# Performance work log

Measured on AMD Instinct MI355X. Metric: run time of the kernel, lower is better.

Reference implementation:

```python
import jax, jax.numpy as jnp
import numpy as np

B, I, R, A, V = 256, 512, 512, 196, 10000

def _linear_params(key, out_dim, in_dim):
    k1, k2 = jax.random.split(key)
    s = 1.0 / np.sqrt(in_dim)
    W = jax.random.uniform(k1, (out_dim, in_dim), minval=-s, maxval=s, dtype=jnp.float32)
    b = jax.random.uniform(k2, (out_dim,), minval=-s, maxval=s, dtype=jnp.float32)
    return W, b

def setup_inputs() -> dict:
    key = jax.random.key(0)
    ks = jax.random.split(key, 16)
    d = {}
    d['x'] = jax.random.normal(ks[0], (B, I), dtype=jnp.float32)
    d['att'] = jax.random.normal(ks[1], (B, A, R), dtype=jnp.float32)
    d['prev_c'] = jax.random.normal(ks[2], (B, R), dtype=jnp.float32)
    d['prev_h'] = jax.random.normal(ks[3], (B, R), dtype=jnp.float32)
    for i, (name, o, inn) in enumerate([('a2a', A, R), ('h2a', A, R), ('d2d', 1, A),
                                         ('i2h', 4 * R, I), ('a2h', 4 * R, R), ('h2h', 4 * R, R),
                                         ('a2a1', A, R), ('h2a1', A, R), ('d2d1', 1, A),
                                         ('proj', V, R)]):
        W, b = _linear_params(ks[4 + i], o, inn)
        d['W_' + name] = W
        d['b_' + name] = b
    return d

def _lin(x, W, b):
    return x @ W.T + b

def _attend(att, h, Wa, ba, Wh, bh, Wd, bd):
    # att: (B, A, R); h: (B, R)
    av = jnp.einsum('bar,or->bao', att, Wa) + ba        # (B, A, A)
    ah = _lin(h, Wh, bh)                                # (B, A)
    dot = jnp.tanh(av + ah[:, :, None])                 # (B, A, A)
    scores = jnp.einsum('bao,o->ba', dot, Wd[0]) + bd[0]  # (B, A)
    w = jax.nn.softmax(scores, axis=-1)
    return jnp.einsum('bar,ba->br', att, w)             # (B, R)

def reference(x, att, prev_c, prev_h,
              W_a2a, b_a2a, W_h2a, b_h2a, W_d2d, b_d2d,
              W_i2h, b_i2h, W_a2h, b_a2h, W_h2h, b_h2h,
              W_a2a1, b_a2a1, W_h2a1, b_h2a1, W_d2d1, b_d2d1,
              W_proj, b_proj):
    # first attention uses prev_h
    prev_att_res = _attend(att, prev_h, W_a2a, b_a2a, W_h2a, b_h2a, W_d2d, b_d2d)
    sums = _lin(x, W_i2h, b_i2h) + _lin(prev_h, W_h2h, b_h2h) + _lin(prev_att_res, W_a2h, b_a2h)
    sig = jax.nn.sigmoid(sums[:, :3 * R])
    in_gate = sig[:, 0:R]
    forget_gate = sig[:, R:2 * R]
    out_gate = sig[:, 2 * R:3 * R]
    in_transform = jnp.tanh(sums[:, 3 * R:4 * R])
    next_c = forget_gate * prev_c + in_gate * in_transform
    next_h = out_gate * jnp.tanh(next_c)
    # second attention uses next_h
    att_res = _attend(att, next_h, W_a2a1, b_a2a1, W_h2a1, b_h2a1, W_d2d1, b_d2d1)
    top_h = att_res + next_h
    logsoft = jax.nn.log_softmax(_lin(top_h, W_proj, b_proj), axis=-1)
    return next_c, top_h, logsoft
```

## Files before the change

kernel.cpp:

```cpp
#include <hip/hip_runtime.h>
#include <math.h>

constexpr int cB  = 256;
constexpr int cI  = 512;
constexpr int cR  = 512;
constexpr int cA  = 196;
constexpr int cV  = 10000;
constexpr int cH4 = 2048;
constexpr int AV2_LD = 200;

typedef short bf16x8 __attribute__((ext_vector_type(8)));
typedef float f32x4  __attribute__((ext_vector_type(4)));
typedef unsigned short us8 __attribute__((ext_vector_type(8)));

__device__ inline unsigned short f2bf(float f) {
    unsigned int u = __float_as_uint(f);
    u += 0x7fffu + ((u >> 16) & 1u);
    return (unsigned short)(u >> 16);
}
__device__ inline float bf2f(unsigned short s) {
    return __uint_as_float(((unsigned int)s) << 16);
}
__device__ inline float tanh_f(float x) {
    return 1.f - 2.f / (1.f + __expf(2.f * x));
}

__global__ __launch_bounds__(256) void k_cvt_ah(
    const float* __restrict__ s0, unsigned short* __restrict__ d0, int nb0,
    const float* __restrict__ s1, unsigned short* __restrict__ d1, int nb1,
    const float* __restrict__ s2, unsigned short* __restrict__ d2, int nb2,
    const float* __restrict__ s3, unsigned short* __restrict__ d3, int nb3,
    const float* __restrict__ h, const float* __restrict__ W,
    const float* __restrict__ bias, float* __restrict__ outah)
{
    __shared__ __align__(16) float h_s[cR];
    int blk = blockIdx.x;
    int ncvt = nb0 + nb1 + nb2 + nb3;
    int t = threadIdx.x;
    if (blk < ncvt) {
        const float* src; unsigned short* dst; int base;
        if (blk < nb0)                  { src = s0; dst = d0; base = blk; }
        else if (blk < nb0 + nb1)       { src = s1; dst = d1; base = blk - nb0; }
        else if (blk < nb0 + nb1 + nb2) { src = s2; dst = d2; base = blk - nb0 - nb1; }
        else                            { src = s3; dst = d3; base = blk - nb0 - nb1 - nb2; }
        int i = base * 256 + t;
        float4 v = ((const float4*)src)[i];
        ushort4 b;
        b.x = f2bf(v.x); b.y = f2bf(v.y); b.z = f2bf(v.z); b.w = f2bf(v.w);
        ((ushort4*)dst)[i] = b;
    } else {
        int b = blk - ncvt;
        h_s[t]       = h[b * cR + t];
        h_s[t + 256] = h[b * cR + t + 256];
        __syncthreads();
        if (t < cA) {
            const float4* Wv = (const float4*)(W + (size_t)t * cR);
            const float4* hv = (const float4*)h_s;
            float acc = 0.f;
            #pragma unroll 4
            for (int k = 0; k < cR / 4; ++k) {
                float4 w4 = Wv[k], x4 = hv[k];
                acc += w4.x * x4.x + w4.y * x4.y + w4.z * x4.z + w4.w * x4.w;
            }
            outah[b * cA + t] = acc + bias[t];
        }
    }
}

__global__ __launch_bounds__(256) void k_ah(
    const float* __restrict__ h, const float* __restrict__ W,
    const float* __restrict__ bias, float* __restrict__ out)
{
    __shared__ __align__(16) float h_s[cR];
    int b = blockIdx.x;
    int t = threadIdx.x;
    h_s[t]       = h[b * cR + t];
    h_s[t + 256] = h[b * cR + t + 256];
    __syncthreads();
    if (t < cA) {
        const float4* Wv = (const float4*)(W + (size_t)t * cR);
        const float4* hv = (const float4*)h_s;
        float acc = 0.f;
        #pragma unroll 4
        for (int k = 0; k < cR / 4; ++k) {
            float4 w4 = Wv[k], x4 = hv[k];
            acc += w4.x * x4.x + w4.y * x4.y + w4.z * x4.z + w4.w * x4.w;
        }
        out[b * cA + t] = acc + bias[t];
    }
}

constexpr int SC_LDA = 72;

__global__ __launch_bounds__(512, 2) void k_scores2g(
    const float* __restrict__ att, unsigned short* __restrict__ att_bf,
    const unsigned short* __restrict__ wa1_bf,
    const unsigned short* __restrict__ wa2_bf,
    const float* __restrict__ ba1, const float* __restrict__ ba2,
    const float* __restrict__ Wd1, const float* __restrict__ bd1,
    const float* __restrict__ ah, float* __restrict__ scores,
    unsigned short* __restrict__ av2)
{
    __shared__ __align__(16) unsigned short att_s[128][SC_LDA];
    __shared__ __align__(16) unsigned short wa_s[448][SC_LDA];
    __shared__ float ba1_s[224];
    __shared__ float ba2_s[224];
    __shared__ float wd_s[224];
    __shared__ float part_s[128][2];

    int tid  = threadIdx.x;
    int wave = tid >> 6;
    int lane = tid & 63;
    int lx   = lane & 15;
    int quad = lane >> 4;
    int mg   = wave >> 2;
    int ng   = wave & 3;
    size_t row0 = (size_t)blockIdx.x * 128;

    if (tid < 224) {
        ba1_s[tid] = (tid < cA) ? ba1[tid] : 0.f;
        ba2_s[tid] = (tid < cA) ? ba2[tid] : 0.f;
        wd_s[tid]  = (tid < cA) ? Wd1[tid] : 0.f;
    }

    int a_r = tid >> 4, a_c = (tid & 15) * 4;
    int w_r = tid >> 3, w_c = (tid & 7) * 8;
    const float* attA = att + (row0 + a_r) * cR + a_c;
    unsigned short* wbA = att_bf + (row0 + a_r) * cR + a_c;

    f32x4 acc[4][7];
    #pragma unroll
    for (int m = 0; m < 4; ++m)
        #pragma unroll
        for (int c = 0; c < 7; ++c) acc[m][c] = (f32x4){0.f, 0.f, 0.f, 0.f};

    float4 patt[4];
    us8    pwa[7];
    #pragma unroll
    for (int i = 0; i < 4; ++i)
        patt[i] = *(const float4*)(attA + (size_t)i * 32 * cR);
    #pragma unroll
    for (int i = 0; i < 7; ++i) {
        int R = w_r + 64 * i;
        const unsigned short* src = (R < 224) ? wa1_bf : wa2_bf;
        int rr = (R < 224) ? R : R - 224;
        pwa[i] = (rr < cA) ? *(const us8*)(src + (size_t)rr * cR + w_c)
                           : (us8){0,0,0,0,0,0,0,0};
    }

    for (int k0 = 0; k0 < cR; k0 += 64) {
        #pragma unroll
        for (int i = 0; i < 4; ++i) {
            float4 v = patt[i];
            ushort4 bv;
            bv.x = f2bf(v.x); bv.y = f2bf(v.y); bv.z = f2bf(v.z); bv.w = f2bf(v.w);
            *(ushort4*)&att_s[a_r + 32 * i][a_c] = bv;
            *(ushort4*)(wbA + (size_t)i * 32 * cR + k0) = bv;
        }
        #pragma unroll
        for (int i = 0; i < 7; ++i)
            *(us8*)&wa_s[w_r + 64 * i][w_c] = pwa[i];
        if (k0 + 64 < cR) {
            #pragma unroll
            for (int i = 0; i < 4; ++i)
                patt[i] = *(const float4*)(attA + (size_t)i * 32 * cR + k0 + 64);
            #pragma unroll
            for (int i = 0; i < 7; ++i) {
                int R = w_r + 64 * i;
                const unsigned short* src = (R < 224) ? wa1_bf : wa2_bf;
                int rr = (R < 224) ? R : R - 224;
                pwa[i] = (rr < cA) ? *(const us8*)(src + (size_t)rr * cR + k0 + 64 + w_c)
                                   : (us8){0,0,0,0,0,0,0,0};
            }
        }
        __syncthreads();
        #pragma unroll
        for (int ks = 0; ks < 2; ++ks) {
            int kb = ks * 32 + quad * 8;
            bf16x8 af[4];
            #pragma unroll
            for (int m = 0; m < 4; ++m)
                af[m] = *(const bf16x8*)&att_s[mg * 64 + m * 16 + lx][kb];
            #pragma unroll
            for (int c = 0; c < 7; ++c) {
                bf16x8 bfr = *(const bf16x8*)&wa_s[ng * 112 + c * 16 + lx][kb];
                #pragma unroll
                for (int m = 0; m < 4; ++m)
                    acc[m][c] = __builtin_amdgcn_mfma_f32_16x16x32_bf16(af[m], bfr, acc[m][c], 0, 0, 0);
            }
        }
        __syncthreads();
    }

    if (ng < 2) {
        #pragma unroll
        for (int m = 0; m < 4; ++m) {
            #pragma unroll
            for (int reg = 0; reg < 4; ++reg) {
                int rl = mg * 64 + m * 16 + quad * 4 + reg;
                float ahv = ah[row0 + rl];
                float part = 0.f;
                #pragma unroll
                for (int c = 0; c < 7; ++c) {
                    int col = ng * 112 + c * 16 + lx;
                    part += tanh_f(acc[m][c][reg] + ba1_s[col] + ahv) * wd_s[col];
                }
                part += __shfl_xor(part, 1);
                part += __shfl_xor(part, 2);
                part += __shfl_xor(part, 4);
                part += __shfl_xor(part, 8);
                if (lx == 0) part_s[rl][ng] = part;
            }
        }
    } else {
        int cb = (ng - 2) * 112;
        #pragma unroll
        for (int m = 0; m < 4; ++m) {
            #pragma unroll
            for (int reg = 0; reg < 4; ++reg) {
                int rl = mg * 64 + m * 16 + quad * 4 + reg;
                size_t ro = (size_t)(row0 + rl) * AV2_LD;
                #pragma unroll
                for (int c = 0; c < 7; ++c) {
                    int col = cb + c * 16 + lx;
                    float v = acc[m][c][reg] + ba2_s[col];
                    if (col < cA)          av2[ro + col] = f2bf(v);
                    else if (col < AV2_LD) av2[ro + col] = 0;
                }
            }
        }
    }
    __syncthreads();
    if (tid < 128)
        scores[row0 + tid] = part_s[tid][0] + part_s[tid][1] + bd1[0];
}

__global__ __launch_bounds__(256) void k_dot2(
    const unsigned short* __restrict__ av2, const float* __restrict__ ah,
    const float* __restrict__ Wd, const float* __restrict__ bd,
    float* __restrict__ scores)
{
    __shared__ float wd_s[AV2_LD];
    int t = threadIdx.x;
    if (t < AV2_LD) wd_s[t] = (t < cA) ? Wd[t] : 0.f;
    __syncthreads();
    int wave = t >> 6, half = (t >> 5) & 1, L = t & 31;
    int r = blockIdx.x * 8 + wave * 2 + half;
    int b = r / cA;
    float s = 0.f;
    if (L < 25) {
        us8 v = *(const us8*)(av2 + (size_t)r * AV2_LD + L * 8);
        const float* ap = ah + (size_t)b * cA + L * 8;
        float4 a0 = *(const float4*)(ap);
        float4 a1 = (L < 24) ? *(const float4*)(ap + 4)
                             : make_float4(0.f, 0.f, 0.f, 0.f);
        float av[8] = {a0.x, a0.y, a0.z, a0.w, a1.x, a1.y, a1.z, a1.w};
        #pragma unroll
        for (int j = 0; j < 8; ++j)
            s += tanh_f(bf2f(v[j]) + av[j]) * wd_s[L * 8 + j];
    }
    s += __shfl_xor(s, 1);
    s += __shfl_xor(s, 2);
    s += __shfl_xor(s, 4);
    s += __shfl_xor(s, 8);
    s += __shfl_xor(s, 16);
    if (L == 0) scores[r] = s + bd[0];
}

__global__ __launch_bounds__(256, 2) void k_scores_cv(
    const float* __restrict__ att, unsigned short* __restrict__ att_bf,
    const unsigned short* __restrict__ wa_bf,
    const float* __restrict__ ba, const float* __restrict__ Wd,
    const float* __restrict__ bd, const float* __restrict__ ah,
    float* __restrict__ scores, int wb)
{
    __shared__ __align__(16) unsigned short att_s[128][SC_LDA];
    __shared__ __align__(16) unsigned short wa_s[224][SC_LDA];
    __shared__ float ba_s[224];
    __shared__ float wd_s[224];
    __shared__ float part_s[128][2];

    int tid  = threadIdx.x;
    int wave = tid >> 6;
    int lane = tid & 63;
    int lx   = lane & 15;
    int quad = lane >> 4;
    int mg   = wave >> 1;
    int ng   = wave & 1;
    size_t row0 = (size_t)blockIdx.x * 128;

    if (tid < 224) {
        ba_s[tid] = (tid < cA) ? ba[tid] : 0.f;
        wd_s[tid] = (tid < cA) ? Wd[tid] : 0.f;
    }

    int a_r = tid >> 4, a_c = (tid & 15) * 4;
    int w_r = tid >> 3, w_c = (tid & 7) * 8;
    const float* attA = att + (row0 + a_r) * cR + a_c;
    unsigned short* wbA = att_bf + (row0 + a_r) * cR + a_c;

    f32x4 acc[4][7];
    #pragma unroll
    for (int m = 0; m < 4; ++m)
        #pragma unroll
        for (int c = 0; c < 7; ++c) acc[m][c] = (f32x4){0.f, 0.f, 0.f, 0.f};

    float4 patt[8];
    us8    pwa[7];
    #pragma unroll
    for (int i = 0; i < 8; ++i)
        patt[i] = *(const float4*)(attA + (size_t)i * 16 * cR);
    #pragma unroll
    for (int i = 0; i < 7; ++i) {
        int r = w_r + 32 * i;
        pwa[i] = (r < cA) ? *(const us8*)(wa_bf + (size_t)r * cR + w_c)
                          : (us8){0,0,0,0,0,0,0,0};
    }

    for (int k0 = 0; k0 < cR; k0 += 64) {
        #pragma unroll
        for (int i = 0; i < 8; ++i) {
            float4 v = patt[i];
            ushort4 bv;
            bv.x = f2bf(v.x); bv.y = f2bf(v.y); bv.z = f2bf(v.z); bv.w = f2bf(v.w);
            *(ushort4*)&att_s[a_r + 16 * i][a_c] = bv;
            if (wb)
                *(ushort4*)(wbA + (size_t)i * 16 * cR + k0) = bv;
        }
        #pragma unroll
        for (int i = 0; i < 7; ++i)
            *(us8*)&wa_s[w_r + 32 * i][w_c] = pwa[i];
        if (k0 + 64 < cR) {
            #pragma unroll
            for (int i = 0; i < 8; ++i)
                patt[i] = *(const float4*)(attA + (size_t)i * 16 * cR + k0 + 64);
            #pragma unroll
            for (int i = 0; i < 7; ++i) {
                int r = w_r + 32 * i;
                pwa[i] = (r < cA) ? *(const us8*)(wa_bf + (size_t)r * cR + k0 + 64 + w_c)
                                  : (us8){0,0,0,0,0,0,0,0};
            }
        }
        __syncthreads();
        #pragma unroll
        for (int ks = 0; ks < 2; ++ks) {
            int kb = ks * 32 + quad * 8;
            bf16x8 af[4];
            #pragma unroll
            for (int m = 0; m < 4; ++m)
                af[m] = *(const bf16x8*)&att_s[mg * 64 + m * 16 + lx][kb];
            #pragma unroll
            for (int c = 0; c < 7; ++c) {
                bf16x8 bfr = *(const bf16x8*)&wa_s[ng * 112 + c * 16 + lx][kb];
                #pragma unroll
                for (int m = 0; m < 4; ++m)
                    acc[m][c] = __builtin_amdgcn_mfma_f32_16x16x32_bf16(af[m], bfr, acc[m][c], 0, 0, 0);
            }
        }
        __syncthreads();
    }

    #pragma unroll
    for (int m = 0; m < 4; ++m) {
        #pragma unroll
        for (int reg = 0; reg < 4; ++reg) {
            int rl = mg * 64 + m * 16 + quad * 4 + reg;
            float ahv = ah[row0 + rl];
            float part = 0.f;
            #pragma unroll
            for (int c = 0; c < 7; ++c) {
                int col = ng * 112 + c * 16 + lx;
                part += tanh_f(acc[m][c][reg] + ba_s[col] + ahv) * wd_s[col];
            }
            part += __shfl_xor(part, 1);
            part += __shfl_xor(part, 2);
            part += __shfl_xor(part, 4);
            part += __shfl_xor(part, 8);
            if (lx == 0) part_s[rl][ng] = part;
        }
    }
    __syncthreads();
    if (tid < 128)
        scores[row0 + tid] = part_s[tid][0] + part_s[tid][1] + bd[0];
}

__global__ __launch_bounds__(256, 2) void k_scores_bf(
    const unsigned short* __restrict__ att_bf,
    const unsigned short* __restrict__ wa_bf,
    const float* __restrict__ ba, const float* __restrict__ Wd,
    const float* __restrict__ bd, const float* __restrict__ ah,
    float* __restrict__ scores)
{
    __shared__ __align__(16) unsigned short att_s[128][SC_LDA];
    __shared__ __align__(16) unsigned short wa_s[224][SC_LDA];
    __shared__ float ba_s[224];
    __shared__ float wd_s[224];
    __shared__ float part_s[128][2];

    int tid  = threadIdx.x;
    int wave = tid >> 6;
    int lane = tid & 63;
    int lx   = lane & 15;
    int quad = lane >> 4;
    int mg   = wave >> 1;
    int ng   = wave & 1;
    size_t row0 = (size_t)blockIdx.x * 128;

    if (tid < 224) {
        ba_s[tid] = (tid < cA) ? ba[tid] : 0.f;
        wd_s[tid] = (tid < cA) ? Wd[tid] : 0.f;
    }

    int a_r = tid >> 3, a_c = (tid & 7) * 8;
    int w_r = tid >> 3, w_c = (tid & 7) * 8;
    const unsigned short* attA = att_bf + (row0 + a_r) * cR + a_c;

    f32x4 acc[4][7];
    #pragma unroll
    for (int m = 0; m < 4; ++m)
        #pragma unroll
        for (int c = 0; c < 7; ++c) acc[m][c] = (f32x4){0.f, 0.f, 0.f, 0.f};

    us8 patt[4];
    us8 pwa[7];
    #pragma unroll
    for (int i = 0; i < 4; ++i)
        patt[i] = *(const us8*)(attA + (size_t)i * 32 * cR);
    #pragma unroll
    for (int i = 0; i < 7; ++i) {
        int r = w_r + 32 * i;
        pwa[i] = (r < cA) ? *(const us8*)(wa_bf + (size_t)r * cR + w_c)
                          : (us8){0,0,0,0,0,0,0,0};
    }

    for (int k0 = 0; k0 < cR; k0 += 64) {
        #pragma unroll
        for (int i = 0; i < 4; ++i)
            *(us8*)&att_s[a_r + 32 * i][a_c] = patt[i];
        #pragma unroll
        for (int i = 0; i < 7; ++i)
            *(us8*)&wa_s[w_r + 32 * i][w_c] = pwa[i];
        if (k0 + 64 < cR) {
            #pragma unroll
            for (int i = 0; i < 4; ++i)
                patt[i] = *(const us8*)(attA + (size_t)i * 32 * cR + k0 + 64);
            #pragma unroll
            for (int i = 0; i < 7; ++i) {
                int r = w_r + 32 * i;
                pwa[i] = (r < cA) ? *(const us8*)(wa_bf + (size_t)r * cR + k0 + 64 + w_c)
                                  : (us8){0,0,0,0,0,0,0,0};
            }
        }
        __syncthreads();
        #pragma unroll
        for (int ks = 0; ks < 2; ++ks) {
            int kb = ks * 32 + quad * 8;
            bf16x8 af[4];
            #pragma unroll
            for (int m = 0; m < 4; ++m)
                af[m] = *(const bf16x8*)&att_s[mg * 64 + m * 16 + lx][kb];
            #pragma unroll
            for (int c = 0; c < 7; ++c) {
                bf16x8 bfr = *(const bf16x8*)&wa_s[ng * 112 + c * 16 + lx][kb];
                #pragma unroll
                for (int m = 0; m < 4; ++m)
                    acc[m][c] = __builtin_amdgcn_mfma_f32_16x16x32_bf16(af[m], bfr, acc[m][c], 0, 0, 0);
            }
        }
        __syncthreads();
    }

    #pragma unroll
    for (int m = 0; m < 4; ++m) {
        #pragma unroll
        for (int reg = 0; reg < 4; ++reg) {
            int rl = mg * 64 + m * 16 + quad * 4 + reg;
            float ahv = ah[row0 + rl];
            float part = 0.f;
            #pragma unroll
            for (int c = 0; c < 7; ++c) {
                int col = ng * 112 + c * 16 + lx;
                part += tanh_f(acc[m][c][reg] + ba_s[col] + ahv) * wd_s[col];
            }
            part += __shfl_xor(part, 1);
            part += __shfl_xor(part, 2);
            part += __shfl_xor(part, 4);
            part += __shfl_xor(part, 8);
            if (lx == 0) part_s[rl][ng] = part;
        }
    }
    __syncthreads();
    if (tid < 128)
        scores[row0 + tid] = part_s[tid][0] + part_s[tid][1] + bd[0];
}

__device__ inline void softmax_w(const float* scores, int b, int t, float* red,
                                 float* w_s)
{
    float s = (t < cA) ? scores[b * cA + t] : -INFINITY;
    red[t] = s; __syncthreads();
    for (int off = 128; off > 0; off >>= 1) {
        if (t < off) red[t] = fmaxf(red[t], red[t + off]);
        __syncthreads();
    }
    float mx = red[0];
    __syncthreads();
    float e = (t < cA) ? __expf(s - mx) : 0.f;
    red[t] = e; __syncthreads();
    for (int off = 128; off > 0; off >>= 1) {
        if (t < off) red[t] += red[t + off];
        __syncthreads();
    }
    float inv = 1.f / red[0];
    if (t < cA) w_s[t] = e * inv;
    __syncthreads();
}

__global__ __launch_bounds__(512) void k_attres_bf(
    const float* __restrict__ scores, const unsigned short* __restrict__ att_bf,
    const float* __restrict__ addin,
    float* __restrict__ out, unsigned short* __restrict__ out_bf)
{
    __shared__ float red[512];
    __shared__ float w_s[cA];
    __shared__ float red2[8][512];
    int b = blockIdx.x, t = threadIdx.x;

    float s = (t < cA) ? scores[b * cA + t] : -INFINITY;
    red[t] = s; __syncthreads();
    for (int off = 256; off > 0; off >>= 1) {
        if (t < off) red[t] = fmaxf(red[t], red[t + off]);
        __syncthreads();
    }
    float mx = red[0];
    __syncthreads();
    float e = (t < cA) ? __expf(s - mx) : 0.f;
    red[t] = e; __syncthreads();
    for (int off = 256; off > 0; off >>= 1) {
        if (t < off) red[t] += red[t + off];
        __syncthreads();
    }
    float inv = 1.f / red[0];
    if (t < cA) w_s[t] = e * inv;
    __syncthreads();

    int p = t >> 6, l = t & 63;
    const unsigned short* base = att_bf + (size_t)b * cA * cR + l * 8;
    float acc[8] = {};
    #pragma unroll 4
    for (int a = p; a < cA; a += 8) {
        us8 v = *(const us8*)(base + (size_t)a * cR);
        float w = w_s[a];
        #pragma unroll
        for (int j = 0; j < 8; ++j)
            acc[j] += bf2f(v[j]) * w;
    }
    #pragma unroll
    for (int j = 0; j < 8; ++j)
        red2[p][l * 8 + j] = acc[j];
    __syncthreads();
    {
        int r = t;
        float s2 = red2[0][r] + red2[1][r] + red2[2][r] + red2[3][r]
                 + red2[4][r] + red2[5][r] + red2[6][r] + red2[7][r];
        if (addin) s2 += addin[b * cR + r];
        out[b * cR + r] = s2;
        out_bf[b * cR + r] = f2bf(s2);
    }
}

__global__ __launch_bounds__(256) void k_attres_f32(
    const float* __restrict__ scores, const float* __restrict__ att,
    const float* __restrict__ addin,
    float* __restrict__ out, unsigned short* __restrict__ out_bf)
{
    __shared__ float red[256];
    __shared__ float w_s[cA];
    int b = blockIdx.x, t = threadIdx.x;
    softmax_w(scores, b, t, red, w_s);

    const float* attb = att + (size_t)b * cA * cR + 2 * t;
    float acc0 = 0.f, acc1 = 0.f;
    #pragma unroll 4
    for (int a = 0; a < cA; ++a) {
        float2 u = *(const float2*)(attb + (size_t)a * cR);
        float w = w_s[a];
        acc0 += u.x * w;
        acc1 += u.y * w;
    }
    if (addin) {
        acc0 += addin[b * cR + 2 * t];
        acc1 += addin[b * cR + 2 * t + 1];
    }
    out[b * cR + 2 * t]     = acc0;
    out[b * cR + 2 * t + 1] = acc1;
    out_bf[b * cR + 2 * t]     = f2bf(acc0);
    out_bf[b * cR + 2 * t + 1] = f2bf(acc1);
}

__global__ __launch_bounds__(256, 4) void k_sums(
    const unsigned short* __restrict__ x_bf,
    const unsigned short* __restrict__ h_bf,
    const unsigned short* __restrict__ ar_bf,
    const float* __restrict__ Wi, const float* __restrict__ Wh,
    const float* __restrict__ Wa,
    const float* __restrict__ bi, const float* __restrict__ bh,
    const float* __restrict__ ba, float* __restrict__ out)
{
    __shared__ __align__(16) unsigned short a_s[32][SC_LDA];
    __shared__ __align__(16) unsigned short w_s[64][SC_LDA];
    int tid  = threadIdx.x;
    int wave = tid >> 6;
    int lane = tid & 63;
    int lx   = lane & 15;
    int quad = lane >> 4;
    int b0 = blockIdx.x * 32;
    int j0 = blockIdx.y * 64;

    const unsigned short* Aarr[3] = {x_bf, h_bf, ar_bf};
    const float* Warr[3] = {Wi, Wh, Wa};

    int a_r = tid >> 3, a_c = (tid & 7) * 8;
    int w_r = tid >> 4, w_c = (tid & 15) * 4;

    f32x4 acc0 = {0.f, 0.f, 0.f, 0.f}, acc1 = {0.f, 0.f, 0.f, 0.f};

    us8 pa;
    float4 pw[4];
    pa = *(const us8*)(Aarr[0] + (size_t)(b0 + a_r) * cR + a_c);
    #pragma unroll
    for (int i = 0; i < 4; ++i)
        pw[i] = *(const float4*)(Warr[0] + (size_t)(j0 + w_r + 16 * i) * cR + w_c);

    for (int it = 0; it < 24; ++it) {
        *(us8*)&a_s[a_r][a_c] = pa;
        #pragma unroll
        for (int i = 0; i < 4; ++i) {
            float4 v = pw[i];
            ushort4 bv;
            bv.x = f2bf(v.x); bv.y = f2bf(v.y); bv.z = f2bf(v.z); bv.w = f2bf(v.w);
            *(ushort4*)&w_s[w_r + 16 * i][w_c] = bv;
        }
        if (it < 23) {
            int s2 = (it + 1) >> 3, k2 = ((it + 1) & 7) * 64;
            pa = *(const us8*)(Aarr[s2] + (size_t)(b0 + a_r) * cR + k2 + a_c);
            #pragma unroll
            for (int i = 0; i < 4; ++i)
                pw[i] = *(const float4*)(Warr[s2] + (size_t)(j0 + w_r + 16 * i) * cR + k2 + w_c);
        }
        __syncthreads();
        #pragma unroll
        for (int ks = 0; ks < 2; ++ks) {
            int kb = ks * 32 + quad * 8;
            bf16x8 afr0 = *(const bf16x8*)&a_s[lx][kb];
            bf16x8 afr1 = *(const bf16x8*)&a_s[16 + lx][kb];
            bf16x8 bfr  = *(const bf16x8*)&w_s[wave * 16 + lx][kb];
            acc0 = __builtin_amdgcn_mfma_f32_16x16x32_bf16(afr0, bfr, acc0, 0, 0, 0);
            acc1 = __builtin_amdgcn_mfma_f32_16x16x32_bf16(afr1, bfr, acc1, 0, 0, 0);
        }
        __syncthreads();
    }
    int j = j0 + wave * 16 + lx;
    float bsum = bi[j] + bh[j] + ba[j];
    #pragma unroll
    for (int reg = 0; reg < 4; ++reg) {
        int b = b0 + quad * 4 + reg;
        out[(size_t)b * cH4 + j]        = acc0[reg] + bsum;
        out[(size_t)(b + 16) * cH4 + j] = acc1[reg] + bsum;
    }
}

__global__ __launch_bounds__(256, 3) void k_lin(
    const unsigned short* __restrict__ in_bf, const float* __restrict__ W,
    const float* __restrict__ bias, float* __restrict__ out, int N)
{
    __shared__ __align__(16) unsigned short a_s[128][SC_LDA];
    __shared__ __align__(16) unsigned short w_s[64][SC_LDA];
    int tid  = threadIdx.x;
    int wave = tid >> 6;
    int lane = tid & 63;
    int lx   = lane & 15;
    int quad = lane >> 4;
    int mg   = wave >> 1;
    int ng   = wave & 1;
    int b0 = blockIdx.x * 128;
    int j0 = blockIdx.y * 64;

    int a_r = tid >> 3, a_c = (tid & 7) * 8;
    int w_r = tid >> 4, w_c = (tid & 15) * 4;

    f32x4 acc[4][2];
    #pragma unroll
    for (int m = 0; m < 4; ++m)
        #pragma unroll
        for (int c = 0; c < 2; ++c) acc[m][c] = (f32x4){0.f, 0.f, 0.f, 0.f};

    us8 pa[4];
    float4 pw[4];
    #pragma unroll
    for (int i = 0; i < 4; ++i)
        pa[i] = *(const us8*)(in_bf + (size_t)(b0 + a_r + 32 * i) * cR + a_c);
    #pragma unroll
    for (int i = 0; i < 4; ++i) {
        int r = j0 + w_r + 16 * i;
        pw[i] = (r < N) ? *(const float4*)(W + (size_t)r * cR + w_c)
                        : make_float4(0.f, 0.f, 0.f, 0.f);
    }

    for (int k0 = 0; k0 < cR; k0 += 64) {
        #pragma unroll
        for (int i = 0; i < 4; ++i)
            *(us8*)&a_s[a_r + 32 * i][a_c] = pa[i];
        #pragma unroll
        for (int i = 0; i < 4; ++i) {
            float4 v = pw[i];
            ushort4 bv;
            bv.x = f2bf(v.x); bv.y = f2bf(v.y); bv.z = f2bf(v.z); bv.w = f2bf(v.w);
            *(ushort4*)&w_s[w_r + 16 * i][w_c] = bv;
        }
        if (k0 + 64 < cR) {
            #pragma unroll
            for (int i = 0; i < 4; ++i)
                pa[i] = *(const us8*)(in_bf + (size_t)(b0 + a_r + 32 * i) * cR + k0 + 64 + a_c);
            #pragma unroll
            for (int i = 0; i < 4; ++i) {
                int r = j0 + w_r + 16 * i;
                pw[i] = (r < N) ? *(const float4*)(W + (size_t)r * cR + k0 + 64 + w_c)
                                : make_float4(0.f, 0.f, 0.f, 0.f);
            }
        }
        __syncthreads();
        #pragma unroll
        for (int ks = 0; ks < 2; ++ks) {
            int kb = ks * 32 + quad * 8;
            bf16x8 af[4];
            #pragma unroll
            for (int m = 0; m < 4; ++m)
                af[m] = *(const bf16x8*)&a_s[mg * 64 + m * 16 + lx][kb];
            #pragma unroll
            for (int c = 0; c < 2; ++c) {
                bf16x8 bfr = *(const bf16x8*)&w_s[ng * 32 + c * 16 + lx][kb];
                #pragma unroll
                for (int m = 0; m < 4; ++m)
                    acc[m][c] = __builtin_amdgcn_mfma_f32_16x16x32_bf16(af[m], bfr, acc[m][c], 0, 0, 0);
            }
        }
        __syncthreads();
    }
    #pragma unroll
    for (int c = 0; c < 2; ++c) {
        int j = j0 + ng * 32 + c * 16 + lx;
        if (j < N) {
            float bv = bias[j];
            #pragma unroll
            for (int m = 0; m < 4; ++m) {
                #pragma unroll
                for (int reg = 0; reg < 4; ++reg) {
                    int b = b0 + mg * 64 + m * 16 + quad * 4 + reg;
                    out[(size_t)b * N + j] = acc[m][c][reg] + bv;
                }
            }
        }
    }
}

__global__ __launch_bounds__(256) void k_cell_ah(
    const float* __restrict__ sums, const float* __restrict__ prev_c,
    const float* __restrict__ W, const float* __restrict__ bias,
    float* __restrict__ next_c, float* __restrict__ next_h,
    float* __restrict__ outah)
{
    __shared__ __align__(16) float h_s[cR];
    int b = blockIdx.x, t = threadIdx.x;
    const float* srow = sums + (size_t)b * cH4;
    #pragma unroll
    for (int rr = 0; rr < 2; ++rr) {
        int j = t + rr * 256;
        float ig = 1.f / (1.f + __expf(-srow[j]));
        float fg = 1.f / (1.f + __expf(-srow[cR + j]));
        float og = 1.f / (1.f + __expf(-srow[2 * cR + j]));
        float gt = tanh_f(srow[3 * cR + j]);
        float c = fg * prev_c[b * cR + j] + ig * gt;
        float h = og * tanh_f(c);
        next_c[b * cR + j] = c;
        next_h[b * cR + j] = h;
        h_s[j] = h;
    }
    __syncthreads();
    if (t < cA) {
        const float4* Wv = (const float4*)(W + (size_t)t * cR);
        const float4* hv = (const float4*)h_s;
        float acc = 0.f;
        #pragma unroll 4
        for (int k = 0; k < cR / 4; ++k) {
            float4 w4 = Wv[k], x4 = hv[k];
            acc += w4.x * x4.x + w4.y * x4.y + w4.z * x4.z + w4.w * x4.w;
        }
        outah[b * cA + t] = acc + bias[t];
    }
}

__global__ __launch_bounds__(256) void k_cell(
    const float* __restrict__ sums, const float* __restrict__ prev_c,
    float* __restrict__ next_c, float* __restrict__ next_h)
{
    int idx = blockIdx.x * 256 + threadIdx.x;
    int b = idx >> 9;
    int j = idx & 511;
    const float* srow = sums + (size_t)b * cH4;
    float ig = 1.f / (1.f + __expf(-srow[j]));
    float fg = 1.f / (1.f + __expf(-srow[cR + j]));
    float og = 1.f / (1.f + __expf(-srow[2 * cR + j]));
    float gt = tanh_f(srow[3 * cR + j]);
    float c = fg * prev_c[idx] + ig * gt;
    float hh = og * tanh_f(c);
    next_c[idx] = c;
    next_h[idx] = hh;
}

__global__ __launch_bounds__(256) void k_logsoftmax(float* __restrict__ logits)
{
    __shared__ float red_m[256];
    __shared__ float red_d[256];
    int b = blockIdx.x, t = threadIdx.x;
    float* row = logits + (size_t)b * cV;
    const float4* row4 = (const float4*)row;
    float m = -INFINITY, d = 0.f;
    for (int v = t; v < cV / 4; v += 256) {
        float4 f = row4[v];
        float m4 = fmaxf(fmaxf(f.x, f.y), fmaxf(f.z, f.w));
        float nm = fmaxf(m, m4);
        d = d * __expf(m - nm) + __expf(f.x - nm) + __expf(f.y - nm)
          + __expf(f.z - nm) + __expf(f.w - nm);
        m = nm;
    }
    red_m[t] = m; red_d[t] = d; __syncthreads();
    for (int off = 128; off > 0; off >>= 1) {
        if (t < off) {
            float m2 = red_m[t + off], d2 = red_d[t + off];
            float M = fmaxf(red_m[t], m2);
            red_d[t] = red_d[t] * __expf(red_m[t] - M) + d2 * __expf(m2 - M);
            red_m[t] = M;
        }
        __syncthreads();
    }
    float lse = red_m[0] + logf(red_d[0]);
    for (int v = t; v < cV / 4; v += 256) {
        float4 f = row4[v];
        f.x -= lse; f.y -= lse; f.z -= lse; f.w -= lse;
        ((float4*)row)[v] = f;
    }
}

extern "C" void kernel_launch(void* const* d_in, const int* in_sizes, int n_in,
                              void* d_out, int out_size, void* d_ws, size_t ws_size,
                              hipStream_t stream)
{
    const float* x      = (const float*)d_in[0];
    const float* att    = (const float*)d_in[1];
    const float* prev_c = (const float*)d_in[2];
    const float* prev_h = (const float*)d_in[3];
    const float* W_a2a  = (const float*)d_in[4];
    const float* b_a2a  = (const float*)d_in[5];
    const float* W_h2a  = (const float*)d_in[6];
    const float* b_h2a  = (const float*)d_in[7];
    const float* W_d2d  = (const float*)d_in[8];
    const float* b_d2d  = (const float*)d_in[9];
    const float* W_i2h  = (const float*)d_in[10];
    const float* b_i2h  = (const float*)d_in[11];
    const float* W_a2h  = (const float*)d_in[12];
    const float* b_a2h  = (const float*)d_in[13];
    const float* W_h2h  = (const float*)d_in[14];
    const float* b_h2h  = (const float*)d_in[15];
    const float* W_a2a1 = (const float*)d_in[16];
    const float* b_a2a1 = (const float*)d_in[17];
    const float* W_h2a1 = (const float*)d_in[18];
    const float* b_h2a1 = (const float*)d_in[19];
    const float* W_d2d1 = (const float*)d_in[20];
    const float* b_d2d1 = (const float*)d_in[21];
    const float* W_proj = (const float*)d_in[22];
    const float* b_proj = (const float*)d_in[23];

    float* out_next_c = (float*)d_out;
    float* out_top_h  = out_next_c + (size_t)cB * cR;
    float* out_logits = out_top_h  + (size_t)cB * cR;

    const size_t ATT_FLOATS = 12845056;
    const size_t AV2_FLOATS = 5017600;
    const size_t NEED_A = (ATT_FLOATS + 1445888) * sizeof(float);
    const size_t NEED_B = (ATT_FLOATS + 1445888 + AV2_FLOATS) * sizeof(float);
    bool bigA = ws_size >= NEED_A;
    bool bigB = ws_size >= NEED_B;

    float* ws = (float*)d_ws;
    unsigned short* att_bf = (unsigned short*)ws;
    float* p = bigA ? (ws + ATT_FLOATS) : ws;
    unsigned short* wa2a_bf  = (unsigned short*)p;  p += 50176;
    unsigned short* wa2a1_bf = (unsigned short*)p;  p += 50176;
    unsigned short* x_bf     = (unsigned short*)p;  p += 65536;
    unsigned short* h_bf     = (unsigned short*)p;  p += 65536;
    unsigned short* ar1_bf   = (unsigned short*)p;  p += 65536;
    unsigned short* ar2_bf   = (unsigned short*)p;  p += 65536;
    unsigned short* toph_bf  = (unsigned short*)p;  p += 65536;
    float* ws_ah      = p;  p += 50176;
    float* ws_scores  = p;  p += 50176;
    float* ws_attres1 = p;  p += 131072;
    float* ws_attres2 = p;  p += 131072;
    float* ws_sums    = p;  p += 524288;
    float* ws_next_h  = p;  p += 131072;
    unsigned short* av2 = (unsigned short*)p;

    k_cvt_ah<<<452 + cB, 256, 0, stream>>>(W_a2a, wa2a_bf, 98,
                                           W_a2a1, wa2a1_bf, 98,
                                           x, x_bf, 128,
                                           prev_h, h_bf, 128,
                                           prev_h, W_h2a, b_h2a, ws_ah);

    if (bigB) {
        k_scores2g<<<(cB * cA) / 128, 512, 0, stream>>>(
            att, att_bf, wa2a_bf, wa2a1_bf, b_a2a, b_a2a1,
            W_d2d, b_d2d, ws_ah, ws_scores, av2);
        k_attres_bf<<<cB, 512, 0, stream>>>(ws_scores, att_bf, nullptr,
                                            ws_attres1, ar1_bf);
        k_sums<<<dim3(8, 32), 256, 0, stream>>>(x_bf, h_bf, ar1_bf,
                                                W_i2h, W_h2h, W_a2h,
                                                b_i2h, b_h2h, b_a2h, ws_sums);
        k_cell_ah<<<cB, 256, 0, stream>>>(ws_sums, prev_c, W_h2a1, b_h2a1,
                                          out_next_c, ws_next_h, ws_ah);
        k_dot2<<<(cB * cA) / 8, 256, 0, stream>>>(av2, ws_ah, W_d2d1, b_d2d1,
                                                  ws_scores);
        k_attres_bf<<<cB, 512, 0, stream>>>(ws_scores, att_bf, ws_next_h,
                                            out_top_h, toph_bf);
    } else if (bigA) {
        k_scores_cv<<<(cB * cA) / 128, 256, 0, stream>>>(att, att_bf, wa2a_bf,
                                                         b_a2a, W_d2d, b_d2d,
                                                         ws_ah, ws_scores, 1);
        k_attres_bf<<<cB, 512, 0, stream>>>(ws_scores, att_bf, nullptr,
                                            ws_attres1, ar1_bf);
        k_sums<<<dim3(8, 32), 256, 0, stream>>>(x_bf, h_bf, ar1_bf,
                                                W_i2h, W_h2h, W_a2h,
                                                b_i2h, b_h2h, b_a2h, ws_sums);
        k_cell_ah<<<cB, 256, 0, stream>>>(ws_sums, prev_c, W_h2a1, b_h2a1,
                                          out_next_c, ws_next_h, ws_ah);
        k_scores_bf<<<(cB * cA) / 128, 256, 0, stream>>>(att_bf, wa2a1_bf,
                                                         b_a2a1, W_d2d1, b_d2d1,
                                                         ws_ah, ws_scores);
        k_attres_bf<<<cB, 512, 0, stream>>>(ws_scores, att_bf, ws_next_h,
                                            out_top_h, toph_bf);
    } else {
        k_scores_cv<<<(cB * cA) / 128, 256, 0, stream>>>(att, att_bf, wa2a_bf,
                                                         b_a2a, W_d2d, b_d2d,
                                                         ws_ah, ws_scores, 0);
        k_attres_f32<<<cB, 256, 0, stream>>>(ws_scores, att, nullptr,
                                             ws_attres1, ar1_bf);
        k_sums<<<dim3(8, 32), 256, 0, stream>>>(x_bf, h_bf, ar1_bf,
                                                W_i2h, W_h2h, W_a2h,
                                                b_i2h, b_h2h, b_a2h, ws_sums);
        k_cell<<<(cB * cR) / 256, 256, 0, stream>>>(ws_sums, prev_c,
                                                    out_next_c, ws_next_h);
        k_ah<<<cB, 256, 0, stream>>>(ws_next_h, W_h2a1, b_h2a1, ws_ah);
        k_scores_cv<<<(cB * cA) / 128, 256, 0, stream>>>(att, att_bf, wa2a1_bf,
                                                         b_a2a1, W_d2d1, b_d2d1,
                                                         ws_ah, ws_scores, 0);
        k_attres_f32<<<cB, 256, 0, stream>>>(ws_scores, att, ws_next_h,
                                             out_top_h, toph_bf);
    }

    k_lin<<<dim3(2, 157), 256, 0, stream>>>(toph_bf, W_proj, b_proj, out_logits, cV);
    k_logsoftmax<<<cB, 256, 0, stream>>>(out_logits);
}
```

Measured before the change: 356.9 us.

## Swizzle scores LDS layout, raise occupancy, pre-convert W_proj to bf16

The k_scores2g LDS tiles lose their padded stride and use an XOR-swizzled 64-wide layout. This cuts the LDS footprint and avoids bank conflicts, so occupancy can go from 2 to 4 blocks per CU. W_proj is also converted to bf16 inside the front conversion kernel when the workspace is large enough, and a new bf16 MFMA projection kernel reads it instead of the fp32 weights. The conversion adds extra blocks to the first kernel and needs more workspace. The higher occupancy target may also force register spilling in the scores kernel.

```diff
diff --git a/kernel.cpp b/kernel.cpp
--- a/kernel.cpp
+++ b/kernel.cpp
@@ -30,19 +30,21 @@
     const float* __restrict__ s1, unsigned short* __restrict__ d1, int nb1,
     const float* __restrict__ s2, unsigned short* __restrict__ d2, int nb2,
     const float* __restrict__ s3, unsigned short* __restrict__ d3, int nb3,
+    const float* __restrict__ s4, unsigned short* __restrict__ d4, int nb4,
     const float* __restrict__ h, const float* __restrict__ W,
     const float* __restrict__ bias, float* __restrict__ outah)
 {
     __shared__ __align__(16) float h_s[cR];
     int blk = blockIdx.x;
-    int ncvt = nb0 + nb1 + nb2 + nb3;
+    int ncvt = nb0 + nb1 + nb2 + nb3 + nb4;
     int t = threadIdx.x;
     if (blk < ncvt) {
         const float* src; unsigned short* dst; int base;
-        if (blk < nb0)                  { src = s0; dst = d0; base = blk; }
-        else if (blk < nb0 + nb1)       { src = s1; dst = d1; base = blk - nb0; }
-        else if (blk < nb0 + nb1 + nb2) { src = s2; dst = d2; base = blk - nb0 - nb1; }
-        else                            { src = s3; dst = d3; base = blk - nb0 - nb1 - nb2; }
+        if (blk < nb0)                        { src = s0; dst = d0; base = blk; }
+        else if (blk < nb0 + nb1)             { src = s1; dst = d1; base = blk - nb0; }
+        else if (blk < nb0 + nb1 + nb2)       { src = s2; dst = d2; base = blk - nb0 - nb1; }
+        else if (blk < nb0 + nb1 + nb2 + nb3) { src = s3; dst = d3; base = blk - nb0 - nb1 - nb2; }
+        else                                  { src = s4; dst = d4; base = blk - nb0 - nb1 - nb2 - nb3; }
         int i = base * 256 + t;
         float4 v = ((const float4*)src)[i];
         ushort4 b;
@@ -92,7 +94,7 @@
 
 constexpr int SC_LDA = 72;
 
-__global__ __launch_bounds__(512, 2) void k_scores2g(
+__global__ __launch_bounds__(512, 4) void k_scores2g(
     const float* __restrict__ att, unsigned short* __restrict__ att_bf,
     const unsigned short* __restrict__ wa1_bf,
     const unsigned short* __restrict__ wa2_bf,
@@ -101,8 +103,8 @@
     const float* __restrict__ ah, float* __restrict__ scores,
     unsigned short* __restrict__ av2)
 {
-    __shared__ __align__(16) unsigned short att_s[128][SC_LDA];
-    __shared__ __align__(16) unsigned short wa_s[448][SC_LDA];
+    __shared__ __align__(16) unsigned short att_s[128 * 64];
+    __shared__ __align__(16) unsigned short wa_s[448 * 64];
     __shared__ float ba1_s[224];
     __shared__ float ba2_s[224];
     __shared__ float wd_s[224];
@@ -154,12 +156,15 @@
             float4 v = patt[i];
             ushort4 bv;
             bv.x = f2bf(v.x); bv.y = f2bf(v.y); bv.z = f2bf(v.z); bv.w = f2bf(v.w);
-            *(ushort4*)&att_s[a_r + 32 * i][a_c] = bv;
+            int r = a_r + 32 * i;
+            *(ushort4*)&att_s[r * 64 + (a_c ^ ((r & 7) * 8))] = bv;
             *(ushort4*)(wbA + (size_t)i * 32 * cR + k0) = bv;
         }
         #pragma unroll
-        for (int i = 0; i < 7; ++i)
-            *(us8*)&wa_s[w_r + 64 * i][w_c] = pwa[i];
+        for (int i = 0; i < 7; ++i) {
+            int r = w_r + 64 * i;
+            *(us8*)&wa_s[r * 64 + (w_c ^ ((r & 7) * 8))] = pwa[i];
+        }
         if (k0 + 64 < cR) {
             #pragma unroll
             for (int i = 0; i < 4; ++i)
@@ -179,11 +184,14 @@
             int kb = ks * 32 + quad * 8;
             bf16x8 af[4];
             #pragma unroll
-            for (int m = 0; m < 4; ++m)
-                af[m] = *(const bf16x8*)&att_s[mg * 64 + m * 16 + lx][kb];
+            for (int m = 0; m < 4; ++m) {
+                int r = mg * 64 + m * 16 + lx;
+                af[m] = *(const bf16x8*)&att_s[r * 64 + (kb ^ ((r & 7) * 8))];
+            }
             #pragma unroll
             for (int c = 0; c < 7; ++c) {
-                bf16x8 bfr = *(const bf16x8*)&wa_s[ng * 112 + c * 16 + lx][kb];
+                int r = ng * 112 + c * 16 + lx;
+                bf16x8 bfr = *(const bf16x8*)&wa_s[r * 64 + (kb ^ ((r & 7) * 8))];
                 #pragma unroll
                 for (int m = 0; m < 4; ++m)
                     acc[m][c] = __builtin_amdgcn_mfma_f32_16x16x32_bf16(af[m], bfr, acc[m][c], 0, 0, 0);
@@ -667,6 +675,96 @@
         int b = b0 + quad * 4 + reg;
         out[(size_t)b * cH4 + j]        = acc0[reg] + bsum;
         out[(size_t)(b + 16) * cH4 + j] = acc1[reg] + bsum;
+    }
+}
+
+__global__ __launch_bounds__(256, 3) void k_lin_bf(
+    const unsigned short* __restrict__ in_bf, const unsigned short* __restrict__ W,
+    const float* __restrict__ bias, float* __restrict__ out, int N)
+{
+    __shared__ __align__(16) unsigned short a_s[128][SC_LDA];
+    __shared__ __align__(16) unsigned short w_s[64][SC_LDA];
+    int tid  = threadIdx.x;
+    int wave = tid >> 6;
+    int lane = tid & 63;
+    int lx   = lane & 15;
+    int quad = lane >> 4;
+    int mg   = wave >> 1;
+    int ng   = wave & 1;
+    int b0 = blockIdx.x * 128;
+    int j0 = blockIdx.y * 64;
+
+    int a_r = tid >> 3, a_c = (tid & 7) * 8;
+    int w_r = tid >> 3, w_c = (tid & 7) * 8;
+
+    f32x4 acc[4][2];
+    #pragma unroll
+    for (int m = 0; m < 4; ++m)
+        #pragma unroll
+        for (int c = 0; c < 2; ++c) acc[m][c] = (f32x4){0.f, 0.f, 0.f, 0.f};
+
+    us8 pa[4];
+    us8 pw[2];
+    #pragma unroll
+    for (int i = 0; i < 4; ++i)
+        pa[i] = *(const us8*)(in_bf + (size_t)(b0 + a_r + 32 * i) * cR + a_c);
+    #pragma unroll
+    for (int i = 0; i < 2; ++i) {
+        int r = j0 + w_r + 32 * i;
+        pw[i] = (r < N) ? *(const us8*)(W + (size_t)r * cR + w_c)
+                        : (us8){0,0,0,0,0,0,0,0};
+    }
+
+    for (int k0 = 0; k0 < cR; k0 += 64) {
+        #pragma unroll
+        for (int i = 0; i < 4; ++i)
+            *(us8*)&a_s[a_r + 32 * i][a_c] = pa[i];
+        #pragma unroll
+        for (int i = 0; i < 2; ++i)
+            *(us8*)&w_s[w_r + 32 * i][w_c] = pw[i];
+        if (k0 + 64 < cR) {
+            #pragma unroll
+            for (int i = 0; i < 4; ++i)
+                pa[i] = *(const us8*)(in_bf + (size_t)(b0 + a_r + 32 * i) * cR + k0 + 64 + a_c);
+            #pragma unroll
+            for (int i = 0; i < 2; ++i) {
+                int r = j0 + w_r + 32 * i;
+                pw[i] = (r < N) ? *(const us8*)(W + (size_t)r * cR + k0 + 64 + w_c)
+                                : (us8){0,0,0,0,0,0,0,0};
+            }
+        }
+        __syncthreads();
+        #pragma unroll
+        for (int ks = 0; ks < 2; ++ks) {
+            int kb = ks * 32 + quad * 8;
+            bf16x8 af[4];
+            #pragma unroll
+            for (int m = 0; m < 4; ++m)
+                af[m] = *(const bf16x8*)&a_s[mg * 64 + m * 16 + lx][kb];
+            #pragma unroll
+            for (int c = 0; c < 2; ++c) {
+                bf16x8 bfr = *(const bf16x8*)&w_s[ng * 32 + c * 16 + lx][kb];
+                #pragma unroll
+                for (int m = 0; m < 4; ++m)
+                    acc[m][c] = __builtin_amdgcn_mfma_f32_16x16x32_bf16(af[m], bfr, acc[m][c], 0, 0, 0);
+            }
+        }
+        __syncthreads();
+    }
+    #pragma unroll
+    for (int c = 0; c < 2; ++c) {
+        int j = j0 + ng * 32 + c * 16 + lx;
+        if (j < N) {
+            float bv = bias[j];
+            #pragma unroll
+            for (int m = 0; m < 4; ++m) {
+                #pragma unroll
+                for (int reg = 0; reg < 4; ++reg) {
+                    int b = b0 + mg * 64 + m * 16 + quad * 4 + reg;
+                    out[(size_t)b * N + j] = acc[m][c][reg] + bv;
+                }
+            }
+        }
     }
 }
 
@@ -885,12 +983,15 @@
     float* out_top_h  = out_next_c + (size_t)cB * cR;
     float* out_logits = out_top_h  + (size_t)cB * cR;
 
-    const size_t ATT_FLOATS = 12845056;
-    const size_t AV2_FLOATS = 5017600;
+    const size_t ATT_FLOATS   = 12845056;
+    const size_t AV2_FLOATS   = 5017600;
+    const size_t WPROJ_FLOATS = 2560000;
     const size_t NEED_A = (ATT_FLOATS + 1445888) * sizeof(float);
     const size_t NEED_B = (ATT_FLOATS + 1445888 + AV2_FLOATS) * sizeof(float);
+    const size_t NEED_C = (ATT_FLOATS + 1445888 + AV2_FLOATS + WPROJ_FLOATS) * sizeof(float);
     bool bigA = ws_size >= NEED_A;
     bool bigB = ws_size >= NEED_B;
+    bool bigC = ws_size >= NEED_C;
 
     float* ws = (float*)d_ws;
     unsigned short* att_bf = (unsigned short*)ws;
@@ -909,12 +1010,16 @@
     float* ws_sums    = p;  p += 524288;
     float* ws_next_h  = p;  p += 131072;
     unsigned short* av2 = (unsigned short*)p;
-
-    k_cvt_ah<<<452 + cB, 256, 0, stream>>>(W_a2a, wa2a_bf, 98,
-                                           W_a2a1, wa2a1_bf, 98,
-                                           x, x_bf, 128,
-                                           prev_h, h_bf, 128,
-                                           prev_h, W_h2a, b_h2a, ws_ah);
+    unsigned short* wproj_bf = (unsigned short*)(p + AV2_FLOATS);
+
+    int nb4 = bigC ? 5000 : 0;
+    k_cvt_ah<<<452 + nb4 + cB, 256, 0, stream>>>(
+        W_a2a, wa2a_bf, 98,
+        W_a2a1, wa2a1_bf, 98,
+        x, x_bf, 128,
+        prev_h, h_bf, 128,
+        W_proj, wproj_bf, nb4,
+        prev_h, W_h2a, b_h2a, ws_ah);
 
     if (bigB) {
         k_scores2g<<<(cB * cA) / 128, 512, 0, stream>>>(
@@ -966,6 +1071,11 @@
                                              out_top_h, toph_bf);
     }
 
-    k_lin<<<dim3(2, 157), 256, 0, stream>>>(toph_bf, W_proj, b_proj, out_logits, cV);
+    if (bigC)
+        k_lin_bf<<<dim3(2, 157), 256, 0, stream>>>(toph_bf, wproj_bf, b_proj,
+                                                   out_logits, cV);
+    else
+        k_lin<<<dim3(2, 157), 256, 0, stream>>>(toph_bf, W_proj, b_proj,
+                                                out_logits, cV);
     k_logsoftmax<<<cB, 256, 0, stream>>>(out_logits);
 }
```

Result: slower. 694.2 us (+94.5%).
